# Optimization experiments

Hardware: AMD Instinct MI355X
Metric: run time of the kernel (lower is better)

## Reference

```python
import jax, jax.numpy as jnp
import numpy as np

B, T, D = 8, 2048, 512


def setup_inputs() -> dict:
    key = jax.random.key(0)
    ks = jax.random.split(key, 12)
    s = 1.0 / np.sqrt(D)
    return {
        "x": jax.random.normal(ks[0], (B, T, D), dtype=jnp.float32),
        "Wq": jax.random.normal(ks[1], (D, D), dtype=jnp.float32) * s,
        "bq": jax.random.normal(ks[2], (D,), dtype=jnp.float32) * 0.01,
        "Wk": jax.random.normal(ks[3], (D, D), dtype=jnp.float32) * s,
        "bk": jax.random.normal(ks[4], (D,), dtype=jnp.float32) * 0.01,
        "Wv": jax.random.normal(ks[5], (D, D), dtype=jnp.float32) * s,
        "bv": jax.random.normal(ks[6], (D,), dtype=jnp.float32) * 0.01,
        "Wbeta": jax.random.normal(ks[7], (1, D), dtype=jnp.float32) * s,
        "bbeta": jax.random.normal(ks[8], (1,), dtype=jnp.float32) * 0.01,
        "Wo": jax.random.normal(ks[9], (D, D), dtype=jnp.float32) * s,
        "bo": jax.random.normal(ks[10], (D,), dtype=jnp.float32) * 0.01,
    }


def _l2_normalize(v, eps=1e-12):
    # torch F.normalize(p=2, dim=-1): v / max(||v||, eps)
    n = jnp.sqrt(jnp.sum(v * v, axis=-1, keepdims=True))
    return v / jnp.maximum(n, eps)


def _deltanet(x, Wq, bq, Wk, bk, Wv, bv, Wbeta, bbeta, Wo, bo):
    Q = x @ Wq.T + bq                      # [B,T,D]
    K = _l2_normalize(x @ Wk.T + bk)       # [B,T,D], unit-norm keys
    V = x @ Wv.T + bv                      # [B,T,D]
    Beta = jax.nn.sigmoid(K @ Wbeta.T + bbeta)  # [B,T,1]

    # time-major for scan: [T,B,D] / [T,B,1]
    Qt = jnp.swapaxes(Q, 0, 1)
    Kt = jnp.swapaxes(K, 0, 1)
    Vt = jnp.swapaxes(V, 0, 1)
    Bt = jnp.swapaxes(Beta, 0, 1)

    S0 = jnp.zeros((x.shape[0], x.shape[-1], x.shape[-1]), dtype=x.dtype)

    def step(S, inp):
        q, k, v, beta = inp                 # [B,D],[B,D],[B,D],[B,1]
        Sk = jnp.einsum("bij,bj->bi", S, k)           # S k_t
        b = beta[:, :, None]                            # [B,1,1]
        # S_t = S - beta (S k) k^T + beta v k^T
        S = S - b * (Sk[:, :, None] * k[:, None, :]) + b * (v[:, :, None] * k[:, None, :])
        o = jnp.einsum("bij,bj->bi", S, q)              # o_t = S_t q_t
        return S, o

    _, Ot = jax.lax.scan(step, S0, (Qt, Kt, Vt, Bt))    # [T,B,D]
    O = jnp.swapaxes(Ot, 0, 1)                          # [B,T,D]
    return O @ Wo.T + bo


def reference(x, Wq, bq, Wk, bk, Wv, bv, Wbeta, bbeta, Wo, bo):
    return _deltanet(x, Wq, bq, Wk, bk, Wv, bv, Wbeta, bbeta, Wo, bo)
```

## Files before the change

### kernel.cpp

```cpp
#include <hip/hip_runtime.h>

#define D 512
#define T 2048
#define BATCH 8
#define M_ROWS (BATCH*T)
#define CHK 64
#define NCHB 32
#define NCHUNK 256

typedef __attribute__((ext_vector_type(8))) short short8;
typedef __attribute__((ext_vector_type(4))) float floatx4;

__device__ __forceinline__ unsigned short f2bf(float f) {
  unsigned int u = __float_as_uint(f);
  u += 0x7FFFu + ((u >> 16) & 1u);
  return (unsigned short)(u >> 16);
}
__device__ __forceinline__ float bf2f(unsigned int h) {
  return __uint_as_float(h << 16);
}
__device__ __forceinline__ float wave_allreduce(float v) {
  #pragma unroll
  for (int m = 32; m; m >>= 1) v += __shfl_xor(v, m, 64);
  return v;
}
__device__ __forceinline__ void unpack8(uint4 r, float f[8]) {
  f[0] = bf2f(r.x & 0xffffu); f[1] = bf2f(r.x >> 16);
  f[2] = bf2f(r.y & 0xffffu); f[3] = bf2f(r.y >> 16);
  f[4] = bf2f(r.z & 0xffffu); f[5] = bf2f(r.z >> 16);
  f[6] = bf2f(r.w & 0xffffu); f[7] = bf2f(r.w >> 16);
}

__global__ __launch_bounds__(256) void cast_kernel(const float* __restrict__ src,
                                                   unsigned short* __restrict__ dst, int n) {
  int idx = (blockIdx.x * 256 + threadIdx.x) * 8;
  if (idx >= n) return;
  const float4* sp = (const float4*)(src + idx);
  float4 a = sp[0], b = sp[1];
  uint4 o;
  o.x = f2bf(a.x) | ((unsigned)f2bf(a.y) << 16);
  o.y = f2bf(a.z) | ((unsigned)f2bf(a.w) << 16);
  o.z = f2bf(b.x) | ((unsigned)f2bf(b.y) << 16);
  o.w = f2bf(b.z) | ((unsigned)f2bf(b.w) << 16);
  *(uint4*)(dst + idx) = o;
}

#define BM 128
#define BN 128
#define BK 32

template<bool OUT_BF16>
__global__ __launch_bounds__(256) void gemm_nt(
    const unsigned short* __restrict__ A, const unsigned short* __restrict__ Bw,
    const float* __restrict__ bias, void* __restrict__ Cout, int M, int N, int K)
{
  __shared__ __align__(16) unsigned short As[BM * BK];
  __shared__ __align__(16) unsigned short Bs[BN * BK];
  int tid  = threadIdx.x;
  int lane = tid & 63;
  int wave = tid >> 6;
  int waveM = (wave >> 1) * 64;
  int waveN = (wave & 1) * 64;
  int lrow = lane & 15;
  int quad = lane >> 4;

  floatx4 acc[4][4];
  #pragma unroll
  for (int a_ = 0; a_ < 4; ++a_)
    #pragma unroll
    for (int b_ = 0; b_ < 4; ++b_) acc[a_][b_] = (floatx4){0.f, 0.f, 0.f, 0.f};

  const unsigned short* Ap = A  + (size_t)(blockIdx.y * BM) * K;
  const unsigned short* Bp = Bw + (size_t)(blockIdx.x * BN) * K;
  int r0 = tid >> 2;
  int c0 = (tid & 3) * 8;

  for (int k0 = 0; k0 < K; k0 += BK) {
    __syncthreads();
    *(uint4*)&As[r0 * BK + c0]        = *(const uint4*)&Ap[(size_t)r0 * K + k0 + c0];
    *(uint4*)&As[(r0 + 64) * BK + c0] = *(const uint4*)&Ap[(size_t)(r0 + 64) * K + k0 + c0];
    *(uint4*)&Bs[r0 * BK + c0]        = *(const uint4*)&Bp[(size_t)r0 * K + k0 + c0];
    *(uint4*)&Bs[(r0 + 64) * BK + c0] = *(const uint4*)&Bp[(size_t)(r0 + 64) * K + k0 + c0];
    __syncthreads();
    short8 af[4], bf[4];
    #pragma unroll
    for (int mt = 0; mt < 4; ++mt)
      af[mt] = *(const short8*)&As[(waveM + mt * 16 + lrow) * BK + quad * 8];
    #pragma unroll
    for (int nt = 0; nt < 4; ++nt)
      bf[nt] = *(const short8*)&Bs[(waveN + nt * 16 + lrow) * BK + quad * 8];
    #pragma unroll
    for (int mt = 0; mt < 4; ++mt)
      #pragma unroll
      for (int nt = 0; nt < 4; ++nt)
        acc[mt][nt] = __builtin_amdgcn_mfma_f32_16x16x32_bf16(af[mt], bf[nt], acc[mt][nt], 0, 0, 0);
  }

  int cm = blockIdx.y * BM + waveM;
  int cn = blockIdx.x * BN + waveN;
  #pragma unroll
  for (int nt = 0; nt < 4; ++nt) {
    int col = cn + nt * 16 + lrow;
    float bv = bias[col];
    #pragma unroll
    for (int mt = 0; mt < 4; ++mt) {
      #pragma unroll
      for (int r = 0; r < 4; ++r) {
        int row = cm + mt * 16 + quad * 4 + r;
        float v = acc[mt][nt][r] + bv;
        if (OUT_BF16) ((unsigned short*)Cout)[(size_t)row * N + col] = f2bf(v);
        else          ((float*)Cout)[(size_t)row * N + col] = v;
      }
    }
  }
}

__global__ __launch_bounds__(256) void norm_beta_kernel(
    unsigned short* __restrict__ Kb, const float* __restrict__ Wbeta,
    const float* __restrict__ bbeta, float* __restrict__ Beta)
{
  int w = blockIdx.x * 4 + (threadIdx.x >> 6);
  int lane = threadIdx.x & 63;
  unsigned short* kp = Kb + (size_t)w * D + lane * 8;
  uint4 raw = *(uint4*)kp;
  float kv[8]; unpack8(raw, kv);
  float ss = 0.f;
  #pragma unroll
  for (int m = 0; m < 8; ++m) ss += kv[m] * kv[m];
  ss = wave_allreduce(ss);
  float inv = 1.0f / fmaxf(sqrtf(ss), 1e-12f);
  const float* wb = Wbeta + lane * 8;
  float dotp = 0.f;
  #pragma unroll
  for (int m = 0; m < 8; ++m) { kv[m] *= inv; dotp += kv[m] * wb[m]; }
  uint4 o;
  o.x = f2bf(kv[0]) | ((unsigned)f2bf(kv[1]) << 16);
  o.y = f2bf(kv[2]) | ((unsigned)f2bf(kv[3]) << 16);
  o.z = f2bf(kv[4]) | ((unsigned)f2bf(kv[5]) << 16);
  o.w = f2bf(kv[6]) | ((unsigned)f2bf(kv[7]) << 16);
  *(uint4*)kp = o;
  dotp = wave_allreduce(dotp);
  if (lane == 0) Beta[w] = 1.0f / (1.0f + expf(-(dotp + bbeta[0])));
}

__global__ __launch_bounds__(256) void transpose_kv(
    const unsigned short* __restrict__ Kb, const unsigned short* __restrict__ Vb,
    unsigned short* __restrict__ KT, unsigned short* __restrict__ VT)
{
  __shared__ __align__(16) unsigned short Kc[64 * 520];
  int cb = blockIdx.x & 255, tid = threadIdx.x;
  const unsigned short* src = (blockIdx.x < 256 ? Kb : Vb) + (size_t)cb * 64 * 512;
  unsigned short* dst = (blockIdx.x < 256 ? KT : VT) + (size_t)cb * 32768;
  #pragma unroll
  for (int it = 0; it < 16; ++it) {
    int e = it * 2048 + tid * 8;
    int row = e >> 9, col = e & 511;
    *(uint4*)&Kc[row * 520 + col] = *(const uint4*)&src[row * 512 + col];
  }
  __syncthreads();
  #pragma unroll
  for (int it = 0; it < 16; ++it) {
    int e = it * 2048 + tid * 8;
    int dk = e >> 6, t0 = e & 63;
    uint4 o;
    unsigned short tv[8];
    #pragma unroll
    for (int u = 0; u < 8; ++u) tv[u] = Kc[(t0 + u) * 520 + dk];
    o.x = tv[0] | ((unsigned)tv[1] << 16);
    o.y = tv[2] | ((unsigned)tv[3] << 16);
    o.z = tv[4] | ((unsigned)tv[5] << 16);
    o.w = tv[6] | ((unsigned)tv[7] << 16);
    *(uint4*)&dst[e] = o;
  }
}

__global__ __launch_bounds__(256) void gram_kernel(
    const unsigned short* __restrict__ Qb, const unsigned short* __restrict__ Kb,
    const float* __restrict__ Beta, float* __restrict__ Abuf,
    unsigned short* __restrict__ Msb)
{
  int cb = blockIdx.x, tid = threadIdx.x, lane = tid & 63, w = tid >> 6;
  int lr = lane & 15, quad = lane >> 4;
  const unsigned short* kc = Kb + (size_t)cb * 64 * 512;
  const unsigned short* qc = Qb + (size_t)cb * 64 * 512;
  floatx4 accK[4], accQ[4];
  #pragma unroll
  for (int nt = 0; nt < 4; ++nt) { accK[nt] = (floatx4){0,0,0,0}; accQ[nt] = (floatx4){0,0,0,0}; }
  #pragma unroll
  for (int ks = 0; ks < 16; ++ks) {
    short8 ak = *(const short8*)&kc[(w * 16 + lr) * 512 + ks * 32 + quad * 8];
    short8 aq = *(const short8*)&qc[(w * 16 + lr) * 512 + ks * 32 + quad * 8];
    short8 bk[4];
    #pragma unroll
    for (int nt = 0; nt < 4; ++nt)
      bk[nt] = *(const short8*)&kc[(nt * 16 + lr) * 512 + ks * 32 + quad * 8];
    #pragma unroll
    for (int nt = 0; nt < 4; ++nt) {
      accK[nt] = __builtin_amdgcn_mfma_f32_16x16x32_bf16(ak, bk[nt], accK[nt], 0, 0, 0);
      accQ[nt] = __builtin_amdgcn_mfma_f32_16x16x32_bf16(aq, bk[nt], accQ[nt], 0, 0, 0);
    }
  }
  #pragma unroll
  for (int nt = 0; nt < 4; ++nt)
    #pragma unroll
    for (int r = 0; r < 4; ++r) {
      int t = w * 16 + quad * 4 + r;
      int j = nt * 16 + lr;
      float bt = Beta[cb * 64 + t];
      Abuf[(size_t)cb * 4096 + t * 64 + j] = (j < t) ? bt * accK[nt][r] : 0.f;
      Msb[(size_t)cb * 4096 + t * 64 + j]  = f2bf((j <= t) ? accQ[nt][r] : 0.f);
    }
}

__global__ __launch_bounds__(64) void tinv_kernel(
    const float* __restrict__ Abuf, const float* __restrict__ Beta,
    unsigned short* __restrict__ Tib)
{
  __shared__ float XT[64 * 68];
  int lane = threadIdx.x;
  int cb = blockIdx.x;
  float bl = Beta[cb * 64 + lane];
  const float* Ab = Abuf + (size_t)cb * 4096;
  unsigned short* To = Tib + (size_t)cb * 4096;
  float* Xr = XT + lane * 68;
  #pragma unroll
  for (int j = 0; j < 68; j += 4) *(float4*)&Xr[j] = (float4){0.f,0.f,0.f,0.f};
  for (int t = 0; t < 64; ++t) {
    const float* Ar = Ab + t * 64;
    float p0 = 0.f, p1 = 0.f, p2 = 0.f, p3 = 0.f;
    for (int jb = 0; jb < t; jb += 4) {
      float4 xv = *(const float4*)&Xr[jb];
      float4 av = *(const float4*)&Ar[jb];
      p0 = fmaf(av.x, xv.x, p0); p1 = fmaf(av.y, xv.y, p1);
      p2 = fmaf(av.z, xv.z, p2); p3 = fmaf(av.w, xv.w, p3);
    }
    float y = ((lane == t) ? 1.f : 0.f) - (p0 + p1) - (p2 + p3);
    Xr[t] = y;
    To[t * 64 + lane] = f2bf(y * bl);
  }
}

__global__ __launch_bounds__(256) void wu_kernel(
    const unsigned short* __restrict__ Tib, const unsigned short* __restrict__ KT,
    const unsigned short* __restrict__ VT, unsigned short* __restrict__ Wneg,
    unsigned short* __restrict__ Ubar)
{
  __shared__ __align__(16) unsigned short WL[64 * 512];
  __shared__ __align__(16) unsigned short UL[64 * 512];
  int cb = blockIdx.x, tid = threadIdx.x, lane = tid & 63, w = tid >> 6;
  int lr = lane & 15, quad = lane >> 4;
  short8 af0 = *(const short8*)&Tib[(size_t)cb * 4096 + (w * 16 + lr) * 64 + quad * 8];
  short8 af1 = *(const short8*)&Tib[(size_t)cb * 4096 + (w * 16 + lr) * 64 + 32 + quad * 8];
  const unsigned short* ktc = KT + (size_t)cb * 32768 + lr * 64 + quad * 8;
  const unsigned short* vtc = VT + (size_t)cb * 32768 + lr * 64 + quad * 8;
  int tbase = w * 16 + quad * 4;
  #pragma unroll 4
  for (int nt = 0; nt < 32; ++nt) {
    short8 bk0 = *(const short8*)(ktc + nt * 1024);
    short8 bk1 = *(const short8*)(ktc + nt * 1024 + 32);
    short8 bv0 = *(const short8*)(vtc + nt * 1024);
    short8 bv1 = *(const short8*)(vtc + nt * 1024 + 32);
    floatx4 z = (floatx4){0.f,0.f,0.f,0.f};
    floatx4 aw = __builtin_amdgcn_mfma_f32_16x16x32_bf16(af0, bk0, z, 0, 0, 0);
    aw = __builtin_amdgcn_mfma_f32_16x16x32_bf16(af1, bk1, aw, 0, 0, 0);
    floatx4 au = __builtin_amdgcn_mfma_f32_16x16x32_bf16(af0, bv0, z, 0, 0, 0);
    au = __builtin_amdgcn_mfma_f32_16x16x32_bf16(af1, bv1, au, 0, 0, 0);
    int bi = nt * 2 + (lr >> 3);
    int lo = lr & 7;
    #pragma unroll
    for (int r = 0; r < 4; ++r) {
      int tt = tbase + r;
      int bis = bi ^ (tt & 7);
      WL[tt * 512 + bis * 8 + lo] = f2bf(-aw[r]);
      UL[tt * 512 + bis * 8 + lo] = f2bf(au[r]);
    }
  }
  __syncthreads();
  unsigned short* wd = Wneg + (size_t)cb * 32768;
  unsigned short* ud = Ubar + (size_t)cb * 32768;
  #pragma unroll
  for (int it = 0; it < 16; ++it) {
    int e = it * 2048 + tid * 8;
    int row = e >> 9, col = e & 511;
    int bis = (col >> 3) ^ (row & 7);
    *(uint4*)&wd[e] = *(const uint4*)&WL[row * 512 + bis * 8];
    *(uint4*)&ud[e] = *(const uint4*)&UL[row * 512 + bis * 8];
  }
}

__global__ __launch_bounds__(256, 1) void seq_kernel(
    const unsigned short* __restrict__ Wneg, const unsigned short* __restrict__ Qb,
    const unsigned short* __restrict__ Ubar, const unsigned short* __restrict__ Msb,
    const unsigned short* __restrict__ KT, unsigned short* __restrict__ Ob)
{
  __shared__ __align__(16) unsigned short Sb[16 * 520];
  __shared__ __align__(16) unsigned short Ut[16 * 72];
  int blk = blockIdx.x;
  int b = blk >> 5, vs = blk & 31;
  int vg0 = vs * 16;
  int tid = threadIdx.x, lane = tid & 63, w = tid >> 6;
  int lr = lane & 15, quad = lane >> 4;

  floatx4 sacc[8];
  #pragma unroll
  for (int nt = 0; nt < 8; ++nt) sacc[nt] = (floatx4){0.f,0.f,0.f,0.f};

  short8 wn[16], qf[16], kt[16], ms[2];
  unsigned short ub[4];

  auto LD_WQ = [&](int cb) {
    const unsigned short* wr = Wneg + ((size_t)cb * 64 + w * 16 + lr) * 512 + quad * 8;
    const unsigned short* qr = Qb   + ((size_t)cb * 64 + w * 16 + lr) * 512 + quad * 8;
    #pragma unroll
    for (int ks = 0; ks < 16; ++ks) {
      wn[ks] = *(const short8*)(wr + ks * 32);
      qf[ks] = *(const short8*)(qr + ks * 32);
    }
  };
  auto LD_KM = [&](int cb) {
    const unsigned short* kr = KT + (size_t)cb * 32768 + (w * 128 + lr) * 64 + quad * 8;
    #pragma unroll
    for (int nt = 0; nt < 8; ++nt) {
      kt[nt * 2 + 0] = *(const short8*)(kr + nt * 1024);
      kt[nt * 2 + 1] = *(const short8*)(kr + nt * 1024 + 32);
    }
    const unsigned short* mr = Msb + (size_t)cb * 4096 + (w * 16 + lr) * 64 + quad * 8;
    ms[0] = *(const short8*)(mr);
    ms[1] = *(const short8*)(mr + 32);
  };
  auto LD_UB = [&](int cb) {
    const unsigned short* ur = Ubar + ((size_t)cb * 64 + w * 16 + quad * 4) * 512 + vg0 + lr;
    #pragma unroll
    for (int r = 0; r < 4; ++r) ub[r] = ur[r * 512];
  };

  int cb0 = b * NCHB;
  LD_WQ(cb0); LD_KM(cb0); LD_UB(cb0);

  for (int ch = 0; ch < NCHB; ++ch) {
    int cb = cb0 + ch;
    int cbn = cb0 + (ch + 1 < NCHB ? ch + 1 : ch);
    #pragma unroll
    for (int nt = 0; nt < 8; ++nt)
      #pragma unroll
      for (int r = 0; r < 4; ++r)
        Sb[(quad * 4 + r) * 520 + w * 128 + nt * 16 + lr] = f2bf(sacc[nt][r]);
    __syncthreads();
    floatx4 du0, du1, do0, do1;
    #pragma unroll
    for (int r = 0; r < 4; ++r) du0[r] = bf2f(ub[r]);
    du1 = (floatx4){0.f,0.f,0.f,0.f};
    do0 = (floatx4){0.f,0.f,0.f,0.f};
    do1 = (floatx4){0.f,0.f,0.f,0.f};
    #pragma unroll
    for (int ks = 0; ks < 16; ++ks) {
      short8 sb = *(const short8*)&Sb[lr * 520 + ks * 32 + quad * 8];
      if (ks & 1) {
        du1 = __builtin_amdgcn_mfma_f32_16x16x32_bf16(wn[ks], sb, du1, 0, 0, 0);
        do1 = __builtin_amdgcn_mfma_f32_16x16x32_bf16(qf[ks], sb, do1, 0, 0, 0);
      } else {
        du0 = __builtin_amdgcn_mfma_f32_16x16x32_bf16(wn[ks], sb, du0, 0, 0, 0);
        do0 = __builtin_amdgcn_mfma_f32_16x16x32_bf16(qf[ks], sb, do0, 0, 0, 0);
      }
    }
    #pragma unroll
    for (int r = 0; r < 4; ++r)
      Ut[lr * 72 + w * 16 + quad * 4 + r] = f2bf(du0[r] + du1[r]);
    LD_WQ(cbn);
    LD_UB(cbn);
    __syncthreads();
    short8 a2_0 = *(const short8*)&Ut[lr * 72 + quad * 8];
    short8 a2_1 = *(const short8*)&Ut[lr * 72 + 32 + quad * 8];
    do0 = __builtin_amdgcn_mfma_f32_16x16x32_bf16(ms[0], a2_0, do0, 0, 0, 0);
    do1 = __builtin_amdgcn_mfma_f32_16x16x32_bf16(ms[1], a2_1, do1, 0, 0, 0);
    #pragma unroll
    for (int nt = 0; nt < 8; ++nt) {
      sacc[nt] = __builtin_amdgcn_mfma_f32_16x16x32_bf16(a2_0, kt[nt * 2 + 0], sacc[nt], 0, 0, 0);
      sacc[nt] = __builtin_amdgcn_mfma_f32_16x16x32_bf16(a2_1, kt[nt * 2 + 1], sacc[nt], 0, 0, 0);
    }
    {
      unsigned short* ob = Ob + ((size_t)cb * 64 + w * 16 + quad * 4) * 512 + vg0 + lr;
      #pragma unroll
      for (int r = 0; r < 4; ++r) ob[r * 512] = f2bf(do0[r] + do1[r]);
    }
    LD_KM(cbn);
  }
}

extern "C" void kernel_launch(void* const* d_in, const int* in_sizes, int n_in,
                              void* d_out, int out_size, void* d_ws, size_t ws_size,
                              hipStream_t stream) {
  const float* x     = (const float*)d_in[0];
  const float* Wq    = (const float*)d_in[1];
  const float* bq    = (const float*)d_in[2];
  const float* Wk    = (const float*)d_in[3];
  const float* bk    = (const float*)d_in[4];
  const float* Wv    = (const float*)d_in[5];
  const float* bv    = (const float*)d_in[6];
  const float* Wbeta = (const float*)d_in[7];
  const float* bbeta = (const float*)d_in[8];
  const float* Wo    = (const float*)d_in[9];
  const float* bo    = (const float*)d_in[10];

  const size_t NE = (size_t)M_ROWS * D;
  const size_t DD = (size_t)D * D;
  unsigned short* Qb  = (unsigned short*)d_ws;
  unsigned short* Kb  = Qb + NE;
  unsigned short* Vb  = Kb + NE;
  unsigned short* Xb  = Vb + NE;
  unsigned short* Wqb = Xb + NE;
  unsigned short* Wkb = Wqb + DD;
  unsigned short* Wvb = Wkb + DD;
  unsigned short* Wob = Wvb + DD;
  float* Beta = (float*)(Wob + DD);
  unsigned short* KT  = (unsigned short*)(Beta + M_ROWS);
  float* Abuf = (float*)(KT + NE);
  unsigned short* Msb = (unsigned short*)(Abuf + (size_t)NCHUNK * 4096);
  unsigned short* Tib = Msb + (size_t)NCHUNK * 4096;
  unsigned short* VT  = Tib + (size_t)NCHUNK * 4096;

  cast_kernel<<<(int)(NE / 2048), 256, 0, stream>>>(x, Xb, (int)NE);
  cast_kernel<<<(int)(DD / 2048), 256, 0, stream>>>(Wq, Wqb, (int)DD);
  cast_kernel<<<(int)(DD / 2048), 256, 0, stream>>>(Wk, Wkb, (int)DD);
  cast_kernel<<<(int)(DD / 2048), 256, 0, stream>>>(Wv, Wvb, (int)DD);
  cast_kernel<<<(int)(DD / 2048), 256, 0, stream>>>(Wo, Wob, (int)DD);

  dim3 gg(D / BN, M_ROWS / BM);
  gemm_nt<true><<<gg, 256, 0, stream>>>(Xb, Wqb, bq, Qb, M_ROWS, D, D);
  gemm_nt<true><<<gg, 256, 0, stream>>>(Xb, Wkb, bk, Kb, M_ROWS, D, D);
  gemm_nt<true><<<gg, 256, 0, stream>>>(Xb, Wvb, bv, Vb, M_ROWS, D, D);

  norm_beta_kernel<<<M_ROWS / 4, 256, 0, stream>>>(Kb, Wbeta, bbeta, Beta);

  transpose_kv<<<2 * NCHUNK, 256, 0, stream>>>(Kb, Vb, KT, VT);
  gram_kernel<<<NCHUNK, 256, 0, stream>>>(Qb, Kb, Beta, Abuf, Msb);
  tinv_kernel<<<NCHUNK, 64, 0, stream>>>(Abuf, Beta, Tib);
  wu_kernel<<<NCHUNK, 256, 0, stream>>>(Tib, KT, VT, Xb, Kb);

  seq_kernel<<<NCHUNK, 256, 0, stream>>>(Xb, Qb, Kb, Msb, KT, Vb);

  gemm_nt<false><<<gg, 256, 0, stream>>>(Vb, Wob, bo, (float*)d_out, M_ROWS, D, D);
}
```

Measured before the change: 478.7 us.

## Widen sequential chunk kernel to 16 waves, use MFMA transpose, prefetch gram loads

The sequential per-chunk scan kernel is reorganized from 4 waves to 16 waves per block. The K dimension is split across 4 wave groups and the partial sums are reduced through shared-memory float buffers, which adds an extra barrier per chunk. This is meant to hide the latency of the serial chunk loop with more parallelism, but it drops the register-level cross-chunk prefetching the old version had. Separately, the K/V transpose now uses identity-matrix MFMAs instead of an LDS transpose, and the gram kernel double-buffers its global loads.

```diff
diff --git a/kernel.cpp b/kernel.cpp
--- a/kernel.cpp
+++ b/kernel.cpp
@@ -147,30 +147,29 @@
     const unsigned short* __restrict__ Kb, const unsigned short* __restrict__ Vb,
     unsigned short* __restrict__ KT, unsigned short* __restrict__ VT)
 {
-  __shared__ __align__(16) unsigned short Kc[64 * 520];
-  int cb = blockIdx.x & 255, tid = threadIdx.x;
+  int cb = blockIdx.x & 255;
   const unsigned short* src = (blockIdx.x < 256 ? Kb : Vb) + (size_t)cb * 64 * 512;
   unsigned short* dst = (blockIdx.x < 256 ? KT : VT) + (size_t)cb * 32768;
-  #pragma unroll
-  for (int it = 0; it < 16; ++it) {
-    int e = it * 2048 + tid * 8;
-    int row = e >> 9, col = e & 511;
-    *(uint4*)&Kc[row * 520 + col] = *(const uint4*)&src[row * 512 + col];
-  }
-  __syncthreads();
-  #pragma unroll
-  for (int it = 0; it < 16; ++it) {
-    int e = it * 2048 + tid * 8;
-    int dk = e >> 6, t0 = e & 63;
-    uint4 o;
-    unsigned short tv[8];
-    #pragma unroll
-    for (int u = 0; u < 8; ++u) tv[u] = Kc[(t0 + u) * 520 + dk];
-    o.x = tv[0] | ((unsigned)tv[1] << 16);
-    o.y = tv[2] | ((unsigned)tv[3] << 16);
-    o.z = tv[4] | ((unsigned)tv[5] << 16);
-    o.w = tv[6] | ((unsigned)tv[7] << 16);
-    *(uint4*)&dst[e] = o;
+  int lane = threadIdx.x & 63, w = threadIdx.x >> 6;
+  int lr = lane & 15, quad = lane >> 4;
+  short8 a0, a1;
+  #pragma unroll
+  for (int j = 0; j < 8; ++j) {
+    a0[j] = (quad == (lr >> 3)     && j == (lr & 7)) ? (short)0x3F80 : (short)0;
+    a1[j] = (quad == 2 + (lr >> 3) && j == (lr & 7)) ? (short)0x3F80 : (short)0;
+  }
+  int t0 = w * 16;
+  #pragma unroll 4
+  for (int dk0 = 0; dk0 < 16; ++dk0) {
+    short8 b = *(const short8*)&src[(size_t)(t0 + lr) * 512 + dk0 * 32 + quad * 8];
+    floatx4 z = (floatx4){0.f,0.f,0.f,0.f};
+    floatx4 c0 = __builtin_amdgcn_mfma_f32_16x16x32_bf16(a0, b, z, 0, 0, 0);
+    floatx4 c1 = __builtin_amdgcn_mfma_f32_16x16x32_bf16(a1, b, z, 0, 0, 0);
+    #pragma unroll
+    for (int r = 0; r < 4; ++r) {
+      dst[(dk0 * 32 +      quad * 4 + r) * 64 + t0 + lr] = f2bf(c0[r]);
+      dst[(dk0 * 32 + 16 + quad * 4 + r) * 64 + t0 + lr] = f2bf(c1[r]);
+    }
   }
 }
 
@@ -186,18 +185,32 @@
   floatx4 accK[4], accQ[4];
   #pragma unroll
   for (int nt = 0; nt < 4; ++nt) { accK[nt] = (floatx4){0,0,0,0}; accQ[nt] = (floatx4){0,0,0,0}; }
+  short8 ak = *(const short8*)&kc[(w * 16 + lr) * 512 + quad * 8];
+  short8 aq = *(const short8*)&qc[(w * 16 + lr) * 512 + quad * 8];
+  short8 bk[4];
+  #pragma unroll
+  for (int nt = 0; nt < 4; ++nt)
+    bk[nt] = *(const short8*)&kc[(nt * 16 + lr) * 512 + quad * 8];
   #pragma unroll
   for (int ks = 0; ks < 16; ++ks) {
-    short8 ak = *(const short8*)&kc[(w * 16 + lr) * 512 + ks * 32 + quad * 8];
-    short8 aq = *(const short8*)&qc[(w * 16 + lr) * 512 + ks * 32 + quad * 8];
-    short8 bk[4];
-    #pragma unroll
-    for (int nt = 0; nt < 4; ++nt)
-      bk[nt] = *(const short8*)&kc[(nt * 16 + lr) * 512 + ks * 32 + quad * 8];
+    short8 akn, aqn, bkn[4];
+    if (ks < 15) {
+      int off = (ks + 1) * 32 + quad * 8;
+      akn = *(const short8*)&kc[(w * 16 + lr) * 512 + off];
+      aqn = *(const short8*)&qc[(w * 16 + lr) * 512 + off];
+      #pragma unroll
+      for (int nt = 0; nt < 4; ++nt)
+        bkn[nt] = *(const short8*)&kc[(nt * 16 + lr) * 512 + off];
+    }
     #pragma unroll
     for (int nt = 0; nt < 4; ++nt) {
       accK[nt] = __builtin_amdgcn_mfma_f32_16x16x32_bf16(ak, bk[nt], accK[nt], 0, 0, 0);
       accQ[nt] = __builtin_amdgcn_mfma_f32_16x16x32_bf16(aq, bk[nt], accQ[nt], 0, 0, 0);
+    }
+    if (ks < 15) {
+      ak = akn; aq = aqn;
+      #pragma unroll
+      for (int nt = 0; nt < 4; ++nt) bk[nt] = bkn[nt];
     }
   }
   #pragma unroll
@@ -288,102 +301,105 @@
   }
 }
 
-__global__ __launch_bounds__(256, 1) void seq_kernel(
+__global__ __launch_bounds__(1024) void seq_kernel(
     const unsigned short* __restrict__ Wneg, const unsigned short* __restrict__ Qb,
     const unsigned short* __restrict__ Ubar, const unsigned short* __restrict__ Msb,
     const unsigned short* __restrict__ KT, unsigned short* __restrict__ Ob)
 {
   __shared__ __align__(16) unsigned short Sb[16 * 520];
+  __shared__ __align__(16) float DUp[64 * 64];
+  __shared__ __align__(16) float DOp[64 * 64];
   __shared__ __align__(16) unsigned short Ut[16 * 72];
   int blk = blockIdx.x;
   int b = blk >> 5, vs = blk & 31;
   int vg0 = vs * 16;
-  int tid = threadIdx.x, lane = tid & 63, w = tid >> 6;
+  int tid = threadIdx.x, lane = tid & 63, wave = tid >> 6;
   int lr = lane & 15, quad = lane >> 4;
-
-  floatx4 sacc[8];
-  #pragma unroll
-  for (int nt = 0; nt < 8; ++nt) sacc[nt] = (floatx4){0.f,0.f,0.f,0.f};
-
-  short8 wn[16], qf[16], kt[16], ms[2];
-  unsigned short ub[4];
-
-  auto LD_WQ = [&](int cb) {
-    const unsigned short* wr = Wneg + ((size_t)cb * 64 + w * 16 + lr) * 512 + quad * 8;
-    const unsigned short* qr = Qb   + ((size_t)cb * 64 + w * 16 + lr) * 512 + quad * 8;
-    #pragma unroll
-    for (int ks = 0; ks < 16; ++ks) {
-      wn[ks] = *(const short8*)(wr + ks * 32);
-      qf[ks] = *(const short8*)(qr + ks * 32);
-    }
-  };
-  auto LD_KM = [&](int cb) {
-    const unsigned short* kr = KT + (size_t)cb * 32768 + (w * 128 + lr) * 64 + quad * 8;
-    #pragma unroll
-    for (int nt = 0; nt < 8; ++nt) {
-      kt[nt * 2 + 0] = *(const short8*)(kr + nt * 1024);
-      kt[nt * 2 + 1] = *(const short8*)(kr + nt * 1024 + 32);
-    }
-    const unsigned short* mr = Msb + (size_t)cb * 4096 + (w * 16 + lr) * 64 + quad * 8;
-    ms[0] = *(const short8*)(mr);
-    ms[1] = *(const short8*)(mr + 32);
-  };
-  auto LD_UB = [&](int cb) {
-    const unsigned short* ur = Ubar + ((size_t)cb * 64 + w * 16 + quad * 4) * 512 + vg0 + lr;
-    #pragma unroll
-    for (int r = 0; r < 4; ++r) ub[r] = ur[r * 512];
-  };
+  int kg = wave & 3;
+  int tm = wave >> 2;
+  int ct = tid >> 4, cv = tid & 15;
+
+  floatx4 sacc[2];
+  sacc[0] = (floatx4){0.f,0.f,0.f,0.f};
+  sacc[1] = (floatx4){0.f,0.f,0.f,0.f};
 
   int cb0 = b * NCHB;
-  LD_WQ(cb0); LD_KM(cb0); LD_UB(cb0);
-
   for (int ch = 0; ch < NCHB; ++ch) {
     int cb = cb0 + ch;
-    int cbn = cb0 + (ch + 1 < NCHB ? ch + 1 : ch);
-    #pragma unroll
-    for (int nt = 0; nt < 8; ++nt)
+    size_t tokb = (size_t)cb * 64;
+    short8 wnf[4], qff[4];
+    {
+      const unsigned short* wr = Wneg + (tokb + tm * 16 + lr) * 512 + kg * 128 + quad * 8;
+      const unsigned short* qr = Qb   + (tokb + tm * 16 + lr) * 512 + kg * 128 + quad * 8;
+      #pragma unroll
+      for (int ks = 0; ks < 4; ++ks) {
+        wnf[ks] = *(const short8*)(wr + ks * 32);
+        qff[ks] = *(const short8*)(qr + ks * 32);
+      }
+    }
+    unsigned short ubv = Ubar[(tokb + ct) * 512 + vg0 + cv];
+    short8 ktf[2][2];
+    {
+      const unsigned short* kr = KT + (size_t)cb * 32768 + (wave * 32 + lr) * 64 + quad * 8;
+      ktf[0][0] = *(const short8*)(kr);
+      ktf[0][1] = *(const short8*)(kr + 32);
+      ktf[1][0] = *(const short8*)(kr + 16 * 64);
+      ktf[1][1] = *(const short8*)(kr + 16 * 64 + 32);
+    }
+    short8 msf0, msf1;
+    if (kg == 0) {
+      const unsigned short* mr = Msb + (size_t)cb * 4096 + (tm * 16 + lr) * 64 + quad * 8;
+      msf0 = *(const short8*)(mr);
+      msf1 = *(const short8*)(mr + 32);
+    }
+    #pragma unroll
+    for (int s = 0; s < 2; ++s)
       #pragma unroll
       for (int r = 0; r < 4; ++r)
-        Sb[(quad * 4 + r) * 520 + w * 128 + nt * 16 + lr] = f2bf(sacc[nt][r]);
+        Sb[(quad * 4 + r) * 520 + wave * 32 + s * 16 + lr] = f2bf(sacc[s][r]);
     __syncthreads();
-    floatx4 du0, du1, do0, do1;
-    #pragma unroll
-    for (int r = 0; r < 4; ++r) du0[r] = bf2f(ub[r]);
-    du1 = (floatx4){0.f,0.f,0.f,0.f};
-    do0 = (floatx4){0.f,0.f,0.f,0.f};
-    do1 = (floatx4){0.f,0.f,0.f,0.f};
-    #pragma unroll
-    for (int ks = 0; ks < 16; ++ks) {
-      short8 sb = *(const short8*)&Sb[lr * 520 + ks * 32 + quad * 8];
-      if (ks & 1) {
-        du1 = __builtin_amdgcn_mfma_f32_16x16x32_bf16(wn[ks], sb, du1, 0, 0, 0);
-        do1 = __builtin_amdgcn_mfma_f32_16x16x32_bf16(qf[ks], sb, do1, 0, 0, 0);
-      } else {
-        du0 = __builtin_amdgcn_mfma_f32_16x16x32_bf16(wn[ks], sb, du0, 0, 0, 0);
-        do0 = __builtin_amdgcn_mfma_f32_16x16x32_bf16(qf[ks], sb, do0, 0, 0, 0);
+    floatx4 du = (floatx4){0.f,0.f,0.f,0.f};
+    floatx4 dq = (floatx4){0.f,0.f,0.f,0.f};
+    #pragma unroll
+    for (int ks = 0; ks < 4; ++ks) {
+      short8 sb = *(const short8*)&Sb[lr * 520 + kg * 128 + ks * 32 + quad * 8];
+      du = __builtin_amdgcn_mfma_f32_16x16x32_bf16(wnf[ks], sb, du, 0, 0, 0);
+      dq = __builtin_amdgcn_mfma_f32_16x16x32_bf16(qff[ks], sb, dq, 0, 0, 0);
+    }
+    #pragma unroll
+    for (int r = 0; r < 4; ++r) {
+      int t = tm * 16 + quad * 4 + r;
+      DUp[t * 64 + lr * 4 + kg] = du[r];
+      DOp[t * 64 + lr * 4 + kg] = dq[r];
+    }
+    __syncthreads();
+    {
+      float4 p = *(const float4*)&DUp[ct * 64 + cv * 4];
+      float uval = (p.x + p.y) + (p.z + p.w) + bf2f(ubv);
+      Ut[cv * 72 + ct] = f2bf(uval);
+    }
+    __syncthreads();
+    short8 a20 = *(const short8*)&Ut[lr * 72 + quad * 8];
+    short8 a21 = *(const short8*)&Ut[lr * 72 + 32 + quad * 8];
+    #pragma unroll
+    for (int s = 0; s < 2; ++s) {
+      sacc[s] = __builtin_amdgcn_mfma_f32_16x16x32_bf16(a20, ktf[s][0], sacc[s], 0, 0, 0);
+      sacc[s] = __builtin_amdgcn_mfma_f32_16x16x32_bf16(a21, ktf[s][1], sacc[s], 0, 0, 0);
+    }
+    if (kg == 0) {
+      floatx4 oo;
+      #pragma unroll
+      for (int r = 0; r < 4; ++r) {
+        int t = tm * 16 + quad * 4 + r;
+        float4 p = *(const float4*)&DOp[t * 64 + lr * 4];
+        oo[r] = (p.x + p.y) + (p.z + p.w);
       }
-    }
-    #pragma unroll
-    for (int r = 0; r < 4; ++r)
-      Ut[lr * 72 + w * 16 + quad * 4 + r] = f2bf(du0[r] + du1[r]);
-    LD_WQ(cbn);
-    LD_UB(cbn);
-    __syncthreads();
-    short8 a2_0 = *(const short8*)&Ut[lr * 72 + quad * 8];
-    short8 a2_1 = *(const short8*)&Ut[lr * 72 + 32 + quad * 8];
-    do0 = __builtin_amdgcn_mfma_f32_16x16x32_bf16(ms[0], a2_0, do0, 0, 0, 0);
-    do1 = __builtin_amdgcn_mfma_f32_16x16x32_bf16(ms[1], a2_1, do1, 0, 0, 0);
-    #pragma unroll
-    for (int nt = 0; nt < 8; ++nt) {
-      sacc[nt] = __builtin_amdgcn_mfma_f32_16x16x32_bf16(a2_0, kt[nt * 2 + 0], sacc[nt], 0, 0, 0);
-      sacc[nt] = __builtin_amdgcn_mfma_f32_16x16x32_bf16(a2_1, kt[nt * 2 + 1], sacc[nt], 0, 0, 0);
-    }
-    {
-      unsigned short* ob = Ob + ((size_t)cb * 64 + w * 16 + quad * 4) * 512 + vg0 + lr;
-      #pragma unroll
-      for (int r = 0; r < 4; ++r) ob[r * 512] = f2bf(do0[r] + do1[r]);
-    }
-    LD_KM(cbn);
+      oo = __builtin_amdgcn_mfma_f32_16x16x32_bf16(msf0, a20, oo, 0, 0, 0);
+      oo = __builtin_amdgcn_mfma_f32_16x16x32_bf16(msf1, a21, oo, 0, 0, 0);
+      unsigned short* ob = Ob + (tokb + tm * 16 + quad * 4) * 512 + vg0 + lr;
+      #pragma unroll
+      for (int r = 0; r < 4; ++r) ob[(size_t)r * 512] = f2bf(oo[r]);
+    }
   }
 }
 
@@ -437,7 +453,7 @@
   tinv_kernel<<<NCHUNK, 64, 0, stream>>>(Abuf, Beta, Tib);
   wu_kernel<<<NCHUNK, 256, 0, stream>>>(Tib, KT, VT, Xb, Kb);
 
-  seq_kernel<<<NCHUNK, 256, 0, stream>>>(Xb, Qb, Kb, Msb, KT, Vb);
+  seq_kernel<<<NCHUNK, 1024, 0, stream>>>(Xb, Qb, Kb, Msb, KT, Vb);
 
   gemm_nt<false><<<gg, 256, 0, stream>>>(Vb, Wob, bo, (float*)d_out, M_ROWS, D, D);
 }
```

Measured after the change: 487.7 us. No clear change (+1.9%).
